# Kernel optimization log

Measured on AMD Instinct MI355X. Metric: run time of the kernel, lower is better.

Reference implementation:

```python
import jax, jax.numpy as jnp
import numpy as np

N_USERS = 100000
N_ITEMS = 50000
NNZ = 1600000
DIM = 128


def setup_inputs() -> dict:
    key = jax.random.key(0)
    ks = jax.random.split(key, 6)
    user_emb = jax.random.normal(ks[0], (N_USERS, DIM), dtype=jnp.float32)
    item_emb = jax.random.normal(ks[1], (N_ITEMS, DIM), dtype=jnp.float32)
    hg_rows = jax.random.randint(ks[2], (NNZ,), 0, N_USERS, dtype=jnp.int32)
    hg_cols = jax.random.randint(ks[3], (NNZ,), 0, N_ITEMS, dtype=jnp.int32)
    hg_vals = jax.random.uniform(ks[4], (NNZ,), dtype=jnp.float32)
    # aggregation: nn.Linear(2*dim, dim) -> weight [dim, 2*dim], bias [dim]
    bound = 1.0 / np.sqrt(2 * DIM)
    W_agg = jax.random.uniform(ks[5], (DIM, 2 * DIM), minval=-bound, maxval=bound, dtype=jnp.float32)
    b_agg = jnp.zeros((DIM,), dtype=jnp.float32)
    return {"user_emb": user_emb, "item_emb": item_emb, "hg_rows": hg_rows,
            "hg_cols": hg_cols, "hg_vals": hg_vals, "W_agg": W_agg, "b_agg": b_agg}


def reference(user_emb, item_emb, hg_rows, hg_cols, hg_vals, W_agg, b_agg):
    n_users = user_emb.shape[0]
    n_items = item_emb.shape[0]
    # node_msg = H @ item_emb  (SpMM via gather + segment_sum)  [n_users, dim]
    gathered = hg_vals[:, None] * item_emb[hg_cols]          # [nnz, dim]
    node_msg = jax.ops.segment_sum(gathered, hg_rows, num_segments=n_users)
    # elementwise gate with user embedding
    edge_node_element = node_msg * user_emb                   # [n_users, dim]
    # msg = Linear(concat([node_msg, gated]))
    cat = jnp.concatenate([node_msg, edge_node_element], axis=1)  # [n_users, 2*dim]
    msg = cat @ W_agg.T + b_agg                               # [n_users, dim]
    # norm_emb = H.T @ msg  (transpose SpMM scatter-back)     [n_items, dim]
    scattered = hg_vals[:, None] * msg[hg_rows]               # [nnz, dim]
    norm_emb = jax.ops.segment_sum(scattered, hg_cols, num_segments=n_items)
    return (norm_emb, msg)
```

## Files before the change

kernel.cpp:

```cpp
#include <hip/hip_runtime.h>

#define DIM 128
#define NB 512

typedef short v8s __attribute__((ext_vector_type(8)));
typedef float v4f __attribute__((ext_vector_type(4)));

__device__ __forceinline__ unsigned short f2bf(float f) {
    unsigned int x = __float_as_uint(f);
    unsigned int r = ((x >> 16) & 1u) + 0x7fffu;
    return (unsigned short)((x + r) >> 16);
}
__device__ __forceinline__ float bf2f(short s) {
    return __uint_as_float(((unsigned)(unsigned short)s) << 16);
}


__global__ __launch_bounds__(256) void k_binA(const int* __restrict__ rows, const int* __restrict__ cols,
                                              int* __restrict__ Mu, int* __restrict__ Mi,
                                              int nnz, int chunk, int nbu, int nbi, int shu, int shi)
{
    __shared__ int hu[256], hi[256];
    int k = blockIdx.x, t = threadIdx.x;
    for (int j = t; j < nbu; j += 256) hu[j] = 0;
    for (int j = t; j < nbi; j += 256) hi[j] = 0;
    __syncthreads();
    int beg = k * chunk, end = min(beg + chunk, nnz);
    if (beg < end) {
        int beg4 = beg >> 2, end4 = end >> 2;
        for (int e4 = beg4 + t; e4 < end4; e4 += 256) {
            int4 r = reinterpret_cast<const int4*>(rows)[e4];
            int4 c = reinterpret_cast<const int4*>(cols)[e4];
            atomicAdd(&hu[r.x >> shu], 1); atomicAdd(&hu[r.y >> shu], 1);
            atomicAdd(&hu[r.z >> shu], 1); atomicAdd(&hu[r.w >> shu], 1);
            atomicAdd(&hi[c.x >> shi], 1); atomicAdd(&hi[c.y >> shi], 1);
            atomicAdd(&hi[c.z >> shi], 1); atomicAdd(&hi[c.w >> shi], 1);
        }
        for (int e = (end4 << 2) + t; e < end; e += 256) {
            atomicAdd(&hu[rows[e] >> shu], 1);
            atomicAdd(&hi[cols[e] >> shi], 1);
        }
    }
    __syncthreads();
    for (int j = t; j < nbu; j += 256) Mu[k * nbu + j] = hu[j];
    for (int j = t; j < nbi; j += 256) Mi[k * nbi + j] = hi[j];
}

__global__ __launch_bounds__(256) void k_binS1(int* __restrict__ M, int* __restrict__ tot,
                                               int nb, int nblk)
{
    __shared__ int ps[256];
    int j = blockIdx.x, t = threadIdx.x;
    int i0 = 2 * t, i1 = 2 * t + 1;
    int v0 = (i0 < nblk) ? M[i0 * nb + j] : 0;
    int v1 = (i1 < nblk) ? M[i1 * nb + j] : 0;
    ps[t] = v0 + v1;
    __syncthreads();
    for (int off = 1; off < 256; off <<= 1) {
        int x = (t >= off) ? ps[t - off] : 0;
        __syncthreads();
        ps[t] += x;
        __syncthreads();
    }
    int ep = ps[t] - (v0 + v1);
    if (i0 < nblk) M[i0 * nb + j] = ep;
    if (i1 < nblk) M[i1 * nb + j] = ep + v0;
    if (t == 255) tot[j] = ps[255];
}

__global__ __launch_bounds__(256) void k_binS2(const int* __restrict__ tot, int* __restrict__ base, int nb)
{
    __shared__ int s[256];
    int t = threadIdx.x;
    int v = (t < nb) ? tot[t] : 0;
    s[t] = v;
    __syncthreads();
    for (int off = 1; off < 256; off <<= 1) {
        int x = (t >= off) ? s[t - off] : 0;
        __syncthreads();
        s[t] += x;
        __syncthreads();
    }
    if (t < nb) base[t] = s[t] - v;
    if (t == 255) base[nb] = s[255];
}

__global__ __launch_bounds__(256) void k_binB(const int* __restrict__ rows, const int* __restrict__ cols,
                                              const float* __restrict__ vals,
                                              const int* __restrict__ Mu, const int* __restrict__ Mi,
                                              const int* __restrict__ base_u, const int* __restrict__ base_i,
                                              int2* __restrict__ bu, int2* __restrict__ bi,
                                              int nnz, int chunk, int nbu, int nbi, int shu, int shi)
{
    __shared__ int cu[256], ci[256];
    int k = blockIdx.x, t = threadIdx.x;
    for (int j = t; j < nbu; j += 256) cu[j] = Mu[k * nbu + j] + base_u[j];
    for (int j = t; j < nbi; j += 256) ci[j] = Mi[k * nbi + j] + base_i[j];
    __syncthreads();
    int mu = (1 << shu) - 1, mi = (1 << shi) - 1;
    int beg = k * chunk, end = min(beg + chunk, nnz);
    if (beg >= end) return;
    int beg4 = beg >> 2, end4 = end >> 2;
    for (int e4 = beg4 + t; e4 < end4; e4 += 256) {
        int4 r = reinterpret_cast<const int4*>(rows)[e4];
        int4 c = reinterpret_cast<const int4*>(cols)[e4];
        int4 v = reinterpret_cast<const int4*>(vals)[e4];
        int p;
        p = atomicAdd(&cu[r.x >> shu], 1); bu[p] = make_int2((c.x << shu) | (r.x & mu), v.x);
        p = atomicAdd(&ci[c.x >> shi], 1); bi[p] = make_int2((r.x << shi) | (c.x & mi), v.x);
        p = atomicAdd(&cu[r.y >> shu], 1); bu[p] = make_int2((c.y << shu) | (r.y & mu), v.y);
        p = atomicAdd(&ci[c.y >> shi], 1); bi[p] = make_int2((r.y << shi) | (c.y & mi), v.y);
        p = atomicAdd(&cu[r.z >> shu], 1); bu[p] = make_int2((c.z << shu) | (r.z & mu), v.z);
        p = atomicAdd(&ci[c.z >> shi], 1); bi[p] = make_int2((r.z << shi) | (c.z & mi), v.z);
        p = atomicAdd(&cu[r.w >> shu], 1); bu[p] = make_int2((c.w << shu) | (r.w & mu), v.w);
        p = atomicAdd(&ci[c.w >> shi], 1); bi[p] = make_int2((r.w << shi) | (c.w & mi), v.w);
    }
    for (int e = (end4 << 2) + t; e < end; e += 256) {
        int r = rows[e], c = cols[e];
        int v = reinterpret_cast<const int*>(vals)[e];
        int p;
        p = atomicAdd(&cu[r >> shu], 1); bu[p] = make_int2((c << shu) | (r & mu), v);
        p = atomicAdd(&ci[c >> shi], 1); bi[p] = make_int2((r << shi) | (c & mi), v);
    }
}

__global__ __launch_bounds__(256) void k_binC(const int2* __restrict__ binned,
                                              const int* __restrict__ base,
                                              int* __restrict__ ptr, int2* __restrict__ cs,
                                              int nrows, int sh, int total)
{
    __shared__ int hist[512];
    __shared__ int scn[512];
    __shared__ int psum[256];
    int j = blockIdx.x, t = threadIdx.x;
    int BR = 1 << sh;
    int row0 = j << sh;
    int beg = base[j], end = base[j + 1];
    for (int r = t; r < BR; r += 256) hist[r] = 0;
    __syncthreads();
    for (int e = beg + t; e < end; e += 256)
        atomicAdd(&hist[binned[e].x & (BR - 1)], 1);
    __syncthreads();
    int v0 = (2 * t < BR) ? hist[2 * t] : 0;
    int v1 = (2 * t + 1 < BR) ? hist[2 * t + 1] : 0;
    psum[t] = v0 + v1;
    __syncthreads();
    for (int off = 1; off < 256; off <<= 1) {
        int x = (t >= off) ? psum[t - off] : 0;
        __syncthreads();
        psum[t] += x;
        __syncthreads();
    }
    int ep = psum[t] - (v0 + v1);
    if (2 * t < BR) scn[2 * t] = ep;
    if (2 * t + 1 < BR) scn[2 * t + 1] = ep + v0;
    __syncthreads();
    for (int r = t; r < BR; r += 256) {
        int row = row0 + r;
        if (row < nrows) ptr[row] = beg + scn[r];
        hist[r] = 0;
    }
    if (j == 0 && t == 0) ptr[nrows] = total;
    __syncthreads();
    for (int e = beg + t; e < end; e += 256) {
        int2 rec = binned[e];
        int rl = rec.x & (BR - 1);
        int pos = beg + scn[rl] + atomicAdd(&hist[rl], 1);
        cs[pos] = make_int2(((unsigned)rec.x) >> sh, rec.y);
    }
}

__global__ void k_tobf(const float* __restrict__ in, unsigned short* __restrict__ out, int n8)
{
    int i = blockIdx.x * 256 + threadIdx.x;
    if (i >= n8) return;
    float4 a = reinterpret_cast<const float4*>(in)[2 * i];
    float4 c = reinterpret_cast<const float4*>(in)[2 * i + 1];
    uint4 o;
    o.x = (unsigned)f2bf(a.x) | ((unsigned)f2bf(a.y) << 16);
    o.y = (unsigned)f2bf(a.z) | ((unsigned)f2bf(a.w) << 16);
    o.z = (unsigned)f2bf(c.x) | ((unsigned)f2bf(c.y) << 16);
    o.w = (unsigned)f2bf(c.z) | ((unsigned)f2bf(c.w) << 16);
    reinterpret_cast<uint4*>(out)[i] = o;
}

__device__ __forceinline__ void gather8(const int2* __restrict__ pairs,
                                        const unsigned short* __restrict__ src,
                                        int beg, int end, int lr, int gb,
                                        float* __restrict__ acc)
{
    for (int base = beg; base < end; base += 8) {
        int2 pl = make_int2(0, 0);
        if (lr < 8 && base + lr < end) pl = pairs[base + lr];
        int   idx[8];
        float vv[8];
        #pragma unroll
        for (int e = 0; e < 8; ++e) {
            idx[e] = __shfl(pl.x, gb + e, 64);
            vv[e]  = __int_as_float(__shfl(pl.y, gb + e, 64));
        }
        v8s s[8];
        #pragma unroll
        for (int e = 0; e < 8; ++e)
            s[e] = *reinterpret_cast<const v8s*>(src + (long long)idx[e] * DIM + 8 * lr);
        #pragma unroll
        for (int e = 0; e < 8; ++e) {
            #pragma unroll
            for (int k = 0; k < 8; ++k)
                acc[k] += vv[e] * bf2f(s[e][k]);
        }
    }
}

__global__ __launch_bounds__(256) void k_spmm_bf(const int* __restrict__ ptr, const int2* __restrict__ pairs,
                                                 const unsigned short* __restrict__ src,
                                                 float* __restrict__ dst, int nrows)
{
    int r = blockIdx.x * 16 + (threadIdx.x >> 4);
    if (r >= nrows) return;
    int lr = threadIdx.x & 15;
    int gb = (threadIdx.x & 63) & ~15;
    int beg = ptr[r], end = ptr[r + 1];
    float acc[8];
    #pragma unroll
    for (int k = 0; k < 8; ++k) acc[k] = 0.f;
    gather8(pairs, src, beg, end, lr, gb, acc);
    float4 o0, o1;
    o0.x = acc[0]; o0.y = acc[1]; o0.z = acc[2]; o0.w = acc[3];
    o1.x = acc[4]; o1.y = acc[5]; o1.z = acc[6]; o1.w = acc[7];
    float* dp = dst + (long long)r * DIM + 8 * lr;
    *reinterpret_cast<float4*>(dp) = o0;
    *reinterpret_cast<float4*>(dp + 4) = o1;
}

__global__ __launch_bounds__(256) void k_spmm4(const int* __restrict__ ptr, const int2* __restrict__ pairs,
                                               const float* __restrict__ src, float* __restrict__ dst, int nrows)
{
    int r = blockIdx.x * 8 + (threadIdx.x >> 5);
    if (r >= nrows) return;
    int l = threadIdx.x & 31;
    int beg = ptr[r], end = ptr[r + 1];
    float4 a0 = {0.f, 0.f, 0.f, 0.f}, a1 = {0.f, 0.f, 0.f, 0.f};
    int j = beg;
    for (; j + 1 < end; j += 2) {
        int2 p0 = pairs[j], p1 = pairs[j + 1];
        float v0 = __int_as_float(p0.y), v1 = __int_as_float(p1.y);
        float4 s0 = *reinterpret_cast<const float4*>(src + (long long)p0.x * DIM + 4 * l);
        float4 s1 = *reinterpret_cast<const float4*>(src + (long long)p1.x * DIM + 4 * l);
        a0.x += v0 * s0.x; a0.y += v0 * s0.y; a0.z += v0 * s0.z; a0.w += v0 * s0.w;
        a1.x += v1 * s1.x; a1.y += v1 * s1.y; a1.z += v1 * s1.z; a1.w += v1 * s1.w;
    }
    if (j < end) {
        int2 p0 = pairs[j];
        float v0 = __int_as_float(p0.y);
        float4 s0 = *reinterpret_cast<const float4*>(src + (long long)p0.x * DIM + 4 * l);
        a0.x += v0 * s0.x; a0.y += v0 * s0.y; a0.z += v0 * s0.z; a0.w += v0 * s0.w;
    }
    a0.x += a1.x; a0.y += a1.y; a0.z += a1.z; a0.w += a1.w;
    *reinterpret_cast<float4*>(dst + (long long)r * DIM + 4 * l) = a0;
}

__global__ void k_bsw(const float* __restrict__ W, unsigned short* __restrict__ Bsw)
{
    int i = blockIdx.x * 256 + threadIdx.x;
    int kt = i >> 12;
    int rem = i & 4095;
    int c = rem >> 5;
    int kk = rem & 31;
    Bsw[i] = f2bf(W[c * 256 + kt * 32 + kk]);
}

__global__ __launch_bounds__(256) void k_fused(const int* __restrict__ ptr,
                                               const int2* __restrict__ pairs,
                                               const unsigned short* __restrict__ itbf,
                                               const float* __restrict__ ue,
                                               const unsigned short* __restrict__ Bsw,
                                               const float* __restrict__ b,
                                               float* __restrict__ msg,
                                               unsigned short* __restrict__ msg_bf, int nu)
{
    __shared__ unsigned short cat[4][16 * 264];
    int tid = threadIdx.x;
    int w = tid >> 6, l = tid & 63;
    int lr = l & 15, hi = l >> 4;
    int gb = l & ~15;
    int d = lr * 8;
    int uw = blockIdx.x * 64 + w * 16;
    unsigned short* mycat = &cat[w][0];

    #pragma unroll
    for (int p = 0; p < 4; ++p) {
        int ur = p * 4 + hi;
        int u = uw + ur;
        float acc[8];
        #pragma unroll
        for (int k = 0; k < 8; ++k) acc[k] = 0.f;
        float4 ue0 = make_float4(0.f,0.f,0.f,0.f), ue1 = make_float4(0.f,0.f,0.f,0.f);
        if (u < nu) {
            ue0 = *reinterpret_cast<const float4*>(ue + (long long)u * DIM + d);
            ue1 = *reinterpret_cast<const float4*>(ue + (long long)u * DIM + d + 4);
            int beg = ptr[u], end = ptr[u + 1];
            gather8(pairs, itbf, beg, end, lr, gb, acc);
        }
        float uev[8] = {ue0.x, ue0.y, ue0.z, ue0.w, ue1.x, ue1.y, ue1.z, ue1.w};
        uint4 nmp, gp;
        nmp.x = (unsigned)f2bf(acc[0]) | ((unsigned)f2bf(acc[1]) << 16);
        nmp.y = (unsigned)f2bf(acc[2]) | ((unsigned)f2bf(acc[3]) << 16);
        nmp.z = (unsigned)f2bf(acc[4]) | ((unsigned)f2bf(acc[5]) << 16);
        nmp.w = (unsigned)f2bf(acc[6]) | ((unsigned)f2bf(acc[7]) << 16);
        gp.x = (unsigned)f2bf(acc[0] * uev[0]) | ((unsigned)f2bf(acc[1] * uev[1]) << 16);
        gp.y = (unsigned)f2bf(acc[2] * uev[2]) | ((unsigned)f2bf(acc[3] * uev[3]) << 16);
        gp.z = (unsigned)f2bf(acc[4] * uev[4]) | ((unsigned)f2bf(acc[5] * uev[5]) << 16);
        gp.w = (unsigned)f2bf(acc[6] * uev[6]) | ((unsigned)f2bf(acc[7] * uev[7]) << 16);
        *reinterpret_cast<uint4*>(mycat + ur * 264 + d) = nmp;
        *reinterpret_cast<uint4*>(mycat + ur * 264 + 128 + d) = gp;
    }
    __syncthreads();

    v4f facc[8];
    #pragma unroll
    for (int ct = 0; ct < 8; ++ct) facc[ct] = (v4f){0.f, 0.f, 0.f, 0.f};
    const unsigned short* arow = mycat + lr * 264;
    for (int kt = 0; kt < 8; ++kt) {
        v8s a = *reinterpret_cast<const v8s*>(arow + kt * 32 + hi * 8);
        #pragma unroll
        for (int ct = 0; ct < 8; ++ct) {
            v8s bb = *reinterpret_cast<const v8s*>(Bsw + kt * 4096 + (ct * 16 + lr) * 32 + hi * 8);
            facc[ct] = __builtin_amdgcn_mfma_f32_16x16x32_bf16(a, bb, facc[ct], 0, 0, 0);
        }
    }

    int ub = uw + hi * 4;
    #pragma unroll
    for (int ct = 0; ct < 8; ++ct) {
        float bc = b[ct * 16 + lr];
        #pragma unroll
        for (int j = 0; j < 4; ++j) {
            int u = ub + j;
            if (u < nu) {
                float val = facc[ct][j] + bc;
                long long p = (long long)u * DIM + ct * 16 + lr;
                msg[p] = val;
                msg_bf[p] = f2bf(val);
            }
        }
    }
}

__global__ __launch_bounds__(256) void k_msg5(const float* __restrict__ nm_in,
                                              const float* __restrict__ ue,
                                              const unsigned short* __restrict__ Bsw,
                                              const float* __restrict__ b,
                                              float* __restrict__ msg,
                                              unsigned short* __restrict__ msg_bf, int nu)
{
    __shared__ unsigned short cat[64 * 264];
    int tid = threadIdx.x;
    int u0 = blockIdx.x * 64;

    for (int idx = tid; idx < 2048; idx += 256) {
        int u = idx >> 5, d4 = idx & 31;
        float4 nm4 = make_float4(0.f, 0.f, 0.f, 0.f);
        float4 ue4 = make_float4(0.f, 0.f, 0.f, 0.f);
        if (u0 + u < nu) {
            long long p = (long long)(u0 + u) * DIM + d4 * 4;
            nm4 = *reinterpret_cast<const float4*>(nm_in + p);
            ue4 = *reinterpret_cast<const float4*>(ue + p);
        }
        unsigned short* row = cat + u * 264;
        uint2 nmp, gp;
        nmp.x = (unsigned)f2bf(nm4.x) | ((unsigned)f2bf(nm4.y) << 16);
        nmp.y = (unsigned)f2bf(nm4.z) | ((unsigned)f2bf(nm4.w) << 16);
        gp.x  = (unsigned)f2bf(nm4.x * ue4.x) | ((unsigned)f2bf(nm4.y * ue4.y) << 16);
        gp.y  = (unsigned)f2bf(nm4.z * ue4.z) | ((unsigned)f2bf(nm4.w * ue4.w) << 16);
        *reinterpret_cast<uint2*>(row + d4 * 4) = nmp;
        *reinterpret_cast<uint2*>(row + 128 + d4 * 4) = gp;
    }
    __syncthreads();

    int l = tid & 63, w = tid >> 6;
    int lr = l & 15, hi = l >> 4;
    v4f acc[8];
    #pragma unroll
    for (int ct = 0; ct < 8; ++ct) acc[ct] = (v4f){0.f, 0.f, 0.f, 0.f};

    const unsigned short* arow = cat + (w * 16 + lr) * 264;
    for (int kt = 0; kt < 8; ++kt) {
        v8s a = *reinterpret_cast<const v8s*>(arow + kt * 32 + hi * 8);
        #pragma unroll
        for (int ct = 0; ct < 8; ++ct) {
            v8s bb = *reinterpret_cast<const v8s*>(Bsw + kt * 4096 + (ct * 16 + lr) * 32 + hi * 8);
            acc[ct] = __builtin_amdgcn_mfma_f32_16x16x32_bf16(a, bb, acc[ct], 0, 0, 0);
        }
    }

    int ub = u0 + w * 16 + hi * 4;
    #pragma unroll
    for (int ct = 0; ct < 8; ++ct) {
        float bc = b[ct * 16 + lr];
        #pragma unroll
        for (int j = 0; j < 4; ++j) {
            int u = ub + j;
            if (u < nu) {
                float val = acc[ct][j] + bc;
                long long p = (long long)u * DIM + ct * 16 + lr;
                msg[p] = val;
                msg_bf[p] = f2bf(val);
            }
        }
    }
}

__global__ void k_wt(const float* __restrict__ W, float* __restrict__ Wt)
{
    int t = blockIdx.x * 256 + threadIdx.x;
    int k = t >> 7;
    int c = t & 127;
    Wt[t] = W[c * 256 + k];
}

#define UPB 32
#define CATP 260

__global__ __launch_bounds__(256) void k_msg4(const float* __restrict__ nm_in,
                                              const float* __restrict__ ue,
                                              const float* __restrict__ Wt,
                                              const float* __restrict__ b,
                                              float* __restrict__ msg, int nu)
{
    __shared__ float cat[UPB * CATP];
    int tid = threadIdx.x;
    int u0 = blockIdx.x * UPB;
    for (int idx = tid; idx < UPB * DIM; idx += 256) {
        int u = idx >> 7, d = idx & 127;
        float nm = 0.f, g = 0.f;
        if (u0 + u < nu) {
            long long p = (long long)(u0 + u) * DIM + d;
            nm = nm_in[p];
            g = nm * ue[p];
        }
        cat[u * CATP + d] = nm;
        cat[u * CATP + DIM + d] = g;
    }
    __syncthreads();

    int tc = tid & 31;
    int tu = tid >> 5;
    float acc[4][4];
    #pragma unroll
    for (int r = 0; r < 4; ++r)
        #pragma unroll
        for (int c = 0; c < 4; ++c) acc[r][c] = 0.f;

    const float* cbase = &cat[(tu * 4) * CATP];
    for (int k4 = 0; k4 < 64; ++k4) {
        float4 w[4];
        #pragma unroll
        for (int kk = 0; kk < 4; ++kk)
            w[kk] = *reinterpret_cast<const float4*>(Wt + (k4 * 4 + kk) * DIM + tc * 4);
        #pragma unroll
        for (int r = 0; r < 4; ++r) {
            float4 a = *reinterpret_cast<const float4*>(cbase + r * CATP + k4 * 4);
            acc[r][0] += a.x * w[0].x + a.y * w[1].x + a.z * w[2].x + a.w * w[3].x;
            acc[r][1] += a.x * w[0].y + a.y * w[1].y + a.z * w[2].y + a.w * w[3].y;
            acc[r][2] += a.x * w[0].z + a.y * w[1].z + a.z * w[2].z + a.w * w[3].z;
            acc[r][3] += a.x * w[0].w + a.y * w[1].w + a.z * w[2].w + a.w * w[3].w;
        }
    }

    float4 bb = *reinterpret_cast<const float4*>(b + tc * 4);
    #pragma unroll
    for (int r = 0; r < 4; ++r) {
        int u = u0 + tu * 4 + r;
        if (u < nu) {
            float4 o;
            o.x = acc[r][0] + bb.x; o.y = acc[r][1] + bb.y;
            o.z = acc[r][2] + bb.z; o.w = acc[r][3] + bb.w;
            *reinterpret_cast<float4*>(msg + (long long)u * DIM + tc * 4) = o;
        }
    }
}


__global__ void k_count(const int* __restrict__ rows, const int* __restrict__ cols,
                        int* __restrict__ cnt_u, int* __restrict__ cnt_i, int nnz4, int nnz)
{
    int i = blockIdx.x * blockDim.x + threadIdx.x;
    int stride = gridDim.x * blockDim.x;
    for (int e4 = i; e4 < nnz4; e4 += stride) {
        int4 r = reinterpret_cast<const int4*>(rows)[e4];
        int4 c = reinterpret_cast<const int4*>(cols)[e4];
        atomicAdd(&cnt_u[r.x], 1); atomicAdd(&cnt_u[r.y], 1);
        atomicAdd(&cnt_u[r.z], 1); atomicAdd(&cnt_u[r.w], 1);
        atomicAdd(&cnt_i[c.x], 1); atomicAdd(&cnt_i[c.y], 1);
        atomicAdd(&cnt_i[c.z], 1); atomicAdd(&cnt_i[c.w], 1);
    }
    for (int e = nnz4 * 4 + i; e < nnz; e += stride) {
        atomicAdd(&cnt_u[rows[e]], 1);
        atomicAdd(&cnt_i[cols[e]], 1);
    }
}

__global__ void k_scan1(const int* __restrict__ cnt, int* __restrict__ ptr,
                        int* __restrict__ partial, int n)
{
    __shared__ int s[256];
    int i = blockIdx.x * 256 + threadIdx.x;
    int v = (i < n) ? cnt[i] : 0;
    s[threadIdx.x] = v;
    __syncthreads();
    for (int off = 1; off < 256; off <<= 1) {
        int x = (threadIdx.x >= off) ? s[threadIdx.x - off] : 0;
        __syncthreads();
        s[threadIdx.x] += x;
        __syncthreads();
    }
    if (i < n) ptr[i] = s[threadIdx.x] - v;
    if (threadIdx.x == 255) partial[blockIdx.x] = s[255];
}

__global__ void k_scan2(int* __restrict__ partial, int n)
{
    __shared__ int s[512];
    int v = (threadIdx.x < (unsigned)n) ? partial[threadIdx.x] : 0;
    s[threadIdx.x] = v;
    __syncthreads();
    for (int off = 1; off < 512; off <<= 1) {
        int x = (threadIdx.x >= off) ? s[threadIdx.x - off] : 0;
        __syncthreads();
        s[threadIdx.x] += x;
        __syncthreads();
    }
    if (threadIdx.x < (unsigned)n) partial[threadIdx.x] = s[threadIdx.x] - v;
}

__global__ void k_scan3(int* __restrict__ ptr, const int* __restrict__ partial,
                        int* __restrict__ woff, int n, int total)
{
    int i = blockIdx.x * 256 + threadIdx.x;
    if (i < n) {
        int p = ptr[i] + partial[blockIdx.x];
        ptr[i] = p;
        woff[i] = p;
        if (i == n - 1) ptr[n] = total;
    }
}

__global__ void k_edge_scatter(const int* __restrict__ rows, const int* __restrict__ cols,
                               const float* __restrict__ vals,
                               int* __restrict__ woff_u, int* __restrict__ woff_i,
                               int2* __restrict__ cs_u, int2* __restrict__ cs_i,
                               int nnz4, int nnz)
{
    int i = blockIdx.x * blockDim.x + threadIdx.x;
    int stride = gridDim.x * blockDim.x;
    for (int e4 = i; e4 < nnz4; e4 += stride) {
        int4 r = reinterpret_cast<const int4*>(rows)[e4];
        int4 c = reinterpret_cast<const int4*>(cols)[e4];
        float4 v = reinterpret_cast<const float4*>(vals)[e4];
        int pu, pi;
        pu = atomicAdd(&woff_u[r.x], 1); cs_u[pu] = make_int2(c.x, __float_as_int(v.x));
        pi = atomicAdd(&woff_i[c.x], 1); cs_i[pi] = make_int2(r.x, __float_as_int(v.x));
        pu = atomicAdd(&woff_u[r.y], 1); cs_u[pu] = make_int2(c.y, __float_as_int(v.y));
        pi = atomicAdd(&woff_i[c.y], 1); cs_i[pi] = make_int2(r.y, __float_as_int(v.y));
        pu = atomicAdd(&woff_u[r.z], 1); cs_u[pu] = make_int2(c.z, __float_as_int(v.z));
        pi = atomicAdd(&woff_i[c.z], 1); cs_i[pi] = make_int2(r.z, __float_as_int(v.z));
        pu = atomicAdd(&woff_u[r.w], 1); cs_u[pu] = make_int2(c.w, __float_as_int(v.w));
        pi = atomicAdd(&woff_i[c.w], 1); cs_i[pi] = make_int2(r.w, __float_as_int(v.w));
    }
    for (int e = nnz4 * 4 + i; e < nnz; e += stride) {
        int r = rows[e], c = cols[e];
        float v = vals[e];
        int pu = atomicAdd(&woff_u[r], 1); cs_u[pu] = make_int2(c, __float_as_int(v));
        int pi = atomicAdd(&woff_i[c], 1); cs_i[pi] = make_int2(r, __float_as_int(v));
    }
}


__global__ void k_scatter(const int* __restrict__ didx, const int* __restrict__ sidx,
                          const float* __restrict__ vals, const float* __restrict__ src,
                          float* __restrict__ dst, long long nnz)
{
    long long t = (long long)blockIdx.x * blockDim.x + threadIdx.x;
    long long total = nnz * 32;
    if (t >= total) return;
    long long e = t >> 5;
    int d = (int)(t & 31) * 4;
    int si = sidx[e];
    int di = didx[e];
    float v = vals[e];
    const float4 s = *reinterpret_cast<const float4*>(src + (long long)si * DIM + d);
    float* p = dst + (long long)di * DIM + d;
    atomicAdd(p + 0, v * s.x);
    atomicAdd(p + 1, v * s.y);
    atomicAdd(p + 2, v * s.z);
    atomicAdd(p + 3, v * s.w);
}

__global__ void k_msg_simple(const float* __restrict__ user_emb, const float* __restrict__ W,
                             const float* __restrict__ b, float* __restrict__ msg)
{
    __shared__ float cat[2 * DIM];
    int u = blockIdx.x;
    int t = threadIdx.x;
    long long base = (long long)u * DIM;
    float nm = msg[base + t];
    float ue = user_emb[base + t];
    cat[t] = nm;
    cat[DIM + t] = nm * ue;
    __syncthreads();
    float acc = b[t];
    const float4* Wr = reinterpret_cast<const float4*>(W + (long long)t * 2 * DIM);
    const float4* c4 = reinterpret_cast<const float4*>(cat);
    #pragma unroll
    for (int k = 0; k < 2 * DIM / 4; ++k) {
        float4 w = Wr[k];
        float4 c = c4[k];
        acc += w.x * c.x + w.y * c.y + w.z * c.z + w.w * c.w;
    }
    msg[base + t] = acc;
}


extern "C" void kernel_launch(void* const* d_in, const int* in_sizes, int n_in,
                              void* d_out, int out_size, void* d_ws, size_t ws_size,
                              hipStream_t stream) {
    const float* user_emb = (const float*)d_in[0];
    const float* item_emb = (const float*)d_in[1];
    const int*   rows     = (const int*)d_in[2];
    const int*   cols     = (const int*)d_in[3];
    const float* vals     = (const float*)d_in[4];
    const float* W        = (const float*)d_in[5];
    const float* b        = (const float*)d_in[6];

    int nu = in_sizes[0] / DIM;
    int ni = in_sizes[1] / DIM;
    int nnz = in_sizes[2];

    float* norm_emb = (float*)d_out;
    float* msg      = (float*)d_out + (long long)ni * DIM;

    auto align256 = [](size_t x) { return (x + 255) & ~(size_t)255; };

    int shu = 0; while ((((long long)nu + (1LL << shu) - 1) >> shu) > 256) shu++;
    int shi = 0; while ((((long long)ni + (1LL << shi) - 1) >> shi) > 256) shi++;
    int nbu = (int)(((long long)nu + (1LL << shu) - 1) >> shu);
    int nbi = (int)(((long long)ni + (1LL << shi) - 1) >> shi);
    int chunk = (((nnz + NB - 1) / NB) + 3) & ~3;

    size_t off = 0;
    size_t o_bu    = off; off = align256(off + (size_t)nnz * 8);
    size_t o_bi    = off; off = align256(off + (size_t)nnz * 8);
    size_t o_csu   = off; off = align256(off + (size_t)nnz * 8);
    size_t o_Mu    = off; off = align256(off + (size_t)NB * nbu * 4);
    size_t o_Mi    = off; off = align256(off + (size_t)NB * nbi * 4);
    size_t o_totu  = off; off = align256(off + (size_t)nbu * 4);
    size_t o_toti  = off; off = align256(off + (size_t)nbi * 4);
    size_t o_baseu = off; off = align256(off + (size_t)(nbu + 1) * 4);
    size_t o_basei = off; off = align256(off + (size_t)(nbi + 1) * 4);
    size_t o_ptru  = off; off = align256(off + (size_t)(nu + 1) * 4);
    size_t o_ptri  = off; off = align256(off + (size_t)(ni + 1) * 4);
    size_t o_bsw   = off; off = align256(off + (size_t)32768 * 2);
    size_t need_base = off;

    size_t itbf_need  = (size_t)ni * DIM * 2;
    size_t msgbf_need = (size_t)nu * DIM * 2;
    bool alias_it = (o_csu - o_bi) >= itbf_need;

    size_t need_fused = need_base;
    size_t o_msgbf_f = need_fused; need_fused = align256(need_fused + msgbf_need);
    size_t o_itbf_f;
    if (alias_it) o_itbf_f = o_bi;
    else { o_itbf_f = need_fused; need_fused = align256(need_fused + itbf_need); }

    size_t need_r9 = need_base;
    bool alias_msg = (o_Mu - o_bi) >= msgbf_need;
    size_t o_itbf_9, o_msgbf_9;
    if (alias_it) o_itbf_9 = o_bi;
    else { o_itbf_9 = need_r9; need_r9 = align256(need_r9 + itbf_need); }
    if (alias_msg) o_msgbf_9 = o_bi;
    else { o_msgbf_9 = need_r9; need_r9 = align256(need_r9 + msgbf_need); }

    bool pack_ok = ((long long)ni < (1LL << (31 - shu))) && ((long long)nu < (1LL << (31 - shi)))
                   && (shu <= 9) && (shi <= 9);

    off = 0;
    size_t o_cs_u   = off; off = align256(off + (size_t)nnz * 8);
    size_t o_cs_i   = off; off = align256(off + (size_t)nnz * 8);
    size_t o_ptr_u  = off; off = align256(off + (size_t)(nu + 1) * 4);
    size_t o_ptr_i  = off; off = align256(off + (size_t)(ni + 1) * 4);
    size_t o_woff_u = off; off = align256(off + (size_t)nu * 4);
    size_t o_woff_i = off; off = align256(off + (size_t)ni * 4);
    size_t o_part_u = off; off = align256(off + 512 * 4);
    size_t o_part_i = off; off = align256(off + 512 * 4);
    size_t o_wt2    = off; off = align256(off + (size_t)256 * DIM * 4);
    size_t need_r5 = off;

    int npb_u = (nu + 255) / 256;
    int npb_i = (ni + 255) / 256;

    char* ws = (char*)d_ws;

    if (pack_ok && (ws_size >= need_fused || ws_size >= need_r9)) {
        bool fused = (ws_size >= need_fused);
        int2* bu     = (int2*)(ws + o_bu);
        int2* bi     = (int2*)(ws + o_bi);
        int2* cs_u   = (int2*)(ws + o_csu);
        int2* cs_i   = (int2*)(ws + o_bu);
        int*  Mu     = (int*)(ws + o_Mu);
        int*  Mi     = (int*)(ws + o_Mi);
        int*  totu   = (int*)(ws + o_totu);
        int*  toti   = (int*)(ws + o_toti);
        int*  baseu  = (int*)(ws + o_baseu);
        int*  basei  = (int*)(ws + o_basei);
        int*  ptr_u  = (int*)(ws + o_ptru);
        int*  ptr_i  = (int*)(ws + o_ptri);
        unsigned short* bsw   = (unsigned short*)(ws + o_bsw);
        unsigned short* itbf  = (unsigned short*)(ws + (fused ? o_itbf_f : o_itbf_9));
        unsigned short* msgbf = (unsigned short*)(ws + (fused ? o_msgbf_f : o_msgbf_9));

        k_binA<<<NB, 256, 0, stream>>>(rows, cols, Mu, Mi, nnz, chunk, nbu, nbi, shu, shi);
        k_bsw<<<128, 256, 0, stream>>>(W, bsw);
        k_binS1<<<nbu, 256, 0, stream>>>(Mu, totu, nbu, NB);
        k_binS1<<<nbi, 256, 0, stream>>>(Mi, toti, nbi, NB);
        k_binS2<<<1, 256, 0, stream>>>(totu, baseu, nbu);
        k_binS2<<<1, 256, 0, stream>>>(toti, basei, nbi);
        k_binB<<<NB, 256, 0, stream>>>(rows, cols, vals, Mu, Mi, baseu, basei,
                                       bu, bi, nnz, chunk, nbu, nbi, shu, shi);
        k_binC<<<nbu, 256, 0, stream>>>(bu, baseu, ptr_u, cs_u, nu, shu, nnz);
        k_binC<<<nbi, 256, 0, stream>>>(bi, basei, ptr_i, cs_i, ni, shi, nnz);

        int n8i = ni * DIM / 8;
        k_tobf<<<(n8i + 255) / 256, 256, 0, stream>>>(item_emb, itbf, n8i);

        if (fused) {
            k_fused<<<(nu + 63) / 64, 256, 0, stream>>>(ptr_u, cs_u, itbf, user_emb,
                                                        bsw, b, msg, msgbf, nu);
        } else {
            k_spmm_bf<<<(nu + 15) / 16, 256, 0, stream>>>(ptr_u, cs_u, itbf, msg, nu);
            k_msg5<<<(nu + 63) / 64, 256, 0, stream>>>(msg, user_emb, bsw, b, msg, msgbf, nu);
        }
        k_spmm_bf<<<(ni + 15) / 16, 256, 0, stream>>>(ptr_i, cs_i, msgbf, norm_emb, ni);
    } else if (ws_size >= need_r5 && npb_u <= 512 && npb_i <= 512) {
        int2*  cs_u   = (int2*)(ws + o_cs_u);
        int2*  cs_i   = (int2*)(ws + o_cs_i);
        int*   ptr_u  = (int*)(ws + o_ptr_u);
        int*   ptr_i  = (int*)(ws + o_ptr_i);
        int*   woff_u = (int*)(ws + o_woff_u);
        int*   woff_i = (int*)(ws + o_woff_i);
        int*   part_u = (int*)(ws + o_part_u);
        int*   part_i = (int*)(ws + o_part_i);
        float* wt     = (float*)(ws + o_wt2);

        hipMemsetAsync(woff_u, 0, (size_t)nu * 4, stream);
        hipMemsetAsync(woff_i, 0, (size_t)ni * 4, stream);

        int nnz4 = nnz / 4;
        int gs = 1024;
        k_count<<<gs, 256, 0, stream>>>(rows, cols, woff_u, woff_i, nnz4, nnz);
        k_wt<<<(256 * DIM) / 256, 256, 0, stream>>>(W, wt);

        k_scan1<<<npb_u, 256, 0, stream>>>(woff_u, ptr_u, part_u, nu);
        k_scan1<<<npb_i, 256, 0, stream>>>(woff_i, ptr_i, part_i, ni);
        k_scan2<<<1, 512, 0, stream>>>(part_u, npb_u);
        k_scan2<<<1, 512, 0, stream>>>(part_i, npb_i);
        k_scan3<<<npb_u, 256, 0, stream>>>(ptr_u, part_u, woff_u, nu, nnz);
        k_scan3<<<npb_i, 256, 0, stream>>>(ptr_i, part_i, woff_i, ni, nnz);

        k_edge_scatter<<<gs, 256, 0, stream>>>(rows, cols, vals, woff_u, woff_i,
                                               cs_u, cs_i, nnz4, nnz);

        k_spmm4<<<(nu + 7) / 8, 256, 0, stream>>>(ptr_u, cs_u, item_emb, msg, nu);
        k_msg4<<<(nu + UPB - 1) / UPB, 256, 0, stream>>>(msg, user_emb, wt, b, msg, nu);
        k_spmm4<<<(ni + 7) / 8, 256, 0, stream>>>(ptr_i, cs_i, msg, norm_emb, ni);
    } else {
        hipMemsetAsync(d_out, 0, (size_t)out_size * sizeof(float), stream);
        long long tot = (long long)nnz * 32;
        int blk = 256;
        long long nblk = (tot + blk - 1) / blk;
        k_scatter<<<(int)nblk, blk, 0, stream>>>(rows, cols, vals, item_emb, msg, nnz);
        k_msg_simple<<<nu, DIM, 0, stream>>>(user_emb, W, b, msg);
        k_scatter<<<(int)nblk, blk, 0, stream>>>(cols, rows, vals, msg, norm_emb, nnz);
    }
}
```

Measured before the change: 266.8 us.

## Gather 16 neighbors per iteration, shrink fused block, pre-convert user embeddings to bf16

The gather helper now loads 16 (index, value) pairs per iteration, using all 16 lanes of each row group, and issues two batches of 8 loads. This halves the loop trips and shuffle overhead per edge. The fused kernel now runs 128-thread blocks covering 32 users, which halves its shared memory and adds more blocks. A new pass converts user embeddings to bf16 in workspace so the fused kernel reads half the bytes, at the cost of an extra full read and write of user_emb and lower gate precision.

```diff
diff --git a/kernel.cpp b/kernel.cpp
--- a/kernel.cpp
+++ b/kernel.cpp
@@ -184,18 +184,18 @@
     reinterpret_cast<uint4*>(out)[i] = o;
 }
 
-__device__ __forceinline__ void gather8(const int2* __restrict__ pairs,
-                                        const unsigned short* __restrict__ src,
-                                        int beg, int end, int lr, int gb,
-                                        float* __restrict__ acc)
-{
-    for (int base = beg; base < end; base += 8) {
+__device__ __forceinline__ void gather16(const int2* __restrict__ pairs,
+                                         const unsigned short* __restrict__ src,
+                                         int beg, int end, int lr, int gb,
+                                         float* __restrict__ acc)
+{
+    for (int base = beg; base < end; base += 16) {
         int2 pl = make_int2(0, 0);
-        if (lr < 8 && base + lr < end) pl = pairs[base + lr];
-        int   idx[8];
-        float vv[8];
-        #pragma unroll
-        for (int e = 0; e < 8; ++e) {
+        if (base + lr < end) pl = pairs[base + lr];
+        int   idx[16];
+        float vv[16];
+        #pragma unroll
+        for (int e = 0; e < 16; ++e) {
             idx[e] = __shfl(pl.x, gb + e, 64);
             vv[e]  = __int_as_float(__shfl(pl.y, gb + e, 64));
         }
@@ -208,6 +208,15 @@
             #pragma unroll
             for (int k = 0; k < 8; ++k)
                 acc[k] += vv[e] * bf2f(s[e][k]);
+        }
+        #pragma unroll
+        for (int e = 0; e < 8; ++e)
+            s[e] = *reinterpret_cast<const v8s*>(src + (long long)idx[8 + e] * DIM + 8 * lr);
+        #pragma unroll
+        for (int e = 0; e < 8; ++e) {
+            #pragma unroll
+            for (int k = 0; k < 8; ++k)
+                acc[k] += vv[8 + e] * bf2f(s[e][k]);
         }
     }
 }
@@ -224,7 +233,7 @@
     float acc[8];
     #pragma unroll
     for (int k = 0; k < 8; ++k) acc[k] = 0.f;
-    gather8(pairs, src, beg, end, lr, gb, acc);
+    gather16(pairs, src, beg, end, lr, gb, acc);
     float4 o0, o1;
     o0.x = acc[0]; o0.y = acc[1]; o0.z = acc[2]; o0.w = acc[3];
     o1.x = acc[4]; o1.y = acc[5]; o1.z = acc[6]; o1.w = acc[7];
@@ -270,22 +279,24 @@
     Bsw[i] = f2bf(W[c * 256 + kt * 32 + kk]);
 }
 
-__global__ __launch_bounds__(256) void k_fused(const int* __restrict__ ptr,
+__global__ __launch_bounds__(128) void k_fused(const int* __restrict__ ptr,
                                                const int2* __restrict__ pairs,
                                                const unsigned short* __restrict__ itbf,
-                                               const float* __restrict__ ue,
+                                               const float* __restrict__ uef32,
+                                               const unsigned short* __restrict__ uebf,
+                                               int use_uebf,
                                                const unsigned short* __restrict__ Bsw,
                                                const float* __restrict__ b,
                                                float* __restrict__ msg,
                                                unsigned short* __restrict__ msg_bf, int nu)
 {
-    __shared__ unsigned short cat[4][16 * 264];
+    __shared__ unsigned short cat[2][16 * 264];
     int tid = threadIdx.x;
     int w = tid >> 6, l = tid & 63;
     int lr = l & 15, hi = l >> 4;
     int gb = l & ~15;
     int d = lr * 8;
-    int uw = blockIdx.x * 64 + w * 16;
+    int uw = blockIdx.x * 32 + w * 16;
     unsigned short* mycat = &cat[w][0];
 
     #pragma unroll
@@ -295,14 +306,25 @@
         float acc[8];
         #pragma unroll
         for (int k = 0; k < 8; ++k) acc[k] = 0.f;
-        float4 ue0 = make_float4(0.f,0.f,0.f,0.f), ue1 = make_float4(0.f,0.f,0.f,0.f);
+        float uev[8];
+        #pragma unroll
+        for (int k = 0; k < 8; ++k) uev[k] = 0.f;
         if (u < nu) {
-            ue0 = *reinterpret_cast<const float4*>(ue + (long long)u * DIM + d);
-            ue1 = *reinterpret_cast<const float4*>(ue + (long long)u * DIM + d + 4);
+            if (use_uebf) {
+                uint4 up = *reinterpret_cast<const uint4*>(uebf + (long long)u * DIM + d);
+                uev[0] = bf2f((short)(up.x & 0xffff)); uev[1] = bf2f((short)(up.x >> 16));
+                uev[2] = bf2f((short)(up.y & 0xffff)); uev[3] = bf2f((short)(up.y >> 16));
+                uev[4] = bf2f((short)(up.z & 0xffff)); uev[5] = bf2f((short)(up.z >> 16));
+                uev[6] = bf2f((short)(up.w & 0xffff)); uev[7] = bf2f((short)(up.w >> 16));
+            } else {
+                float4 ue0 = *reinterpret_cast<const float4*>(uef32 + (long long)u * DIM + d);
+                float4 ue1 = *reinterpret_cast<const float4*>(uef32 + (long long)u * DIM + d + 4);
+                uev[0] = ue0.x; uev[1] = ue0.y; uev[2] = ue0.z; uev[3] = ue0.w;
+                uev[4] = ue1.x; uev[5] = ue1.y; uev[6] = ue1.z; uev[7] = ue1.w;
+            }
             int beg = ptr[u], end = ptr[u + 1];
-            gather8(pairs, itbf, beg, end, lr, gb, acc);
-        }
-        float uev[8] = {ue0.x, ue0.y, ue0.z, ue0.w, ue1.x, ue1.y, ue1.z, ue1.w};
+            gather16(pairs, itbf, beg, end, lr, gb, acc);
+        }
         uint4 nmp, gp;
         nmp.x = (unsigned)f2bf(acc[0]) | ((unsigned)f2bf(acc[1]) << 16);
         nmp.y = (unsigned)f2bf(acc[2]) | ((unsigned)f2bf(acc[3]) << 16);
@@ -665,6 +687,7 @@
 
     size_t itbf_need  = (size_t)ni * DIM * 2;
     size_t msgbf_need = (size_t)nu * DIM * 2;
+    size_t uebf_need  = (size_t)nu * DIM * 2;
     bool alias_it = (o_csu - o_bi) >= itbf_need;
 
     size_t need_fused = need_base;
@@ -672,6 +695,8 @@
     size_t o_itbf_f;
     if (alias_it) o_itbf_f = o_bi;
     else { o_itbf_f = need_fused; need_fused = align256(need_fused + itbf_need); }
+    size_t o_uebf = need_fused;
+    size_t need_fused_ue = align256(need_fused + uebf_need);
 
     size_t need_r9 = need_base;
     bool alias_msg = (o_Mu - o_bi) >= msgbf_need;
@@ -702,7 +727,8 @@
     char* ws = (char*)d_ws;
 
     if (pack_ok && (ws_size >= need_fused || ws_size >= need_r9)) {
-        bool fused = (ws_size >= need_fused);
+        bool fused   = (ws_size >= need_fused);
+        bool use_ue  = fused && (ws_size >= need_fused_ue);
         int2* bu     = (int2*)(ws + o_bu);
         int2* bi     = (int2*)(ws + o_bi);
         int2* cs_u   = (int2*)(ws + o_csu);
@@ -718,9 +744,14 @@
         unsigned short* bsw   = (unsigned short*)(ws + o_bsw);
         unsigned short* itbf  = (unsigned short*)(ws + (fused ? o_itbf_f : o_itbf_9));
         unsigned short* msgbf = (unsigned short*)(ws + (fused ? o_msgbf_f : o_msgbf_9));
+        unsigned short* uebf  = (unsigned short*)(ws + o_uebf);
 
         k_binA<<<NB, 256, 0, stream>>>(rows, cols, Mu, Mi, nnz, chunk, nbu, nbi, shu, shi);
         k_bsw<<<128, 256, 0, stream>>>(W, bsw);
+        if (use_ue) {
+            int n8u = nu * DIM / 8;
+            k_tobf<<<(n8u + 255) / 256, 256, 0, stream>>>(user_emb, uebf, n8u);
+        }
         k_binS1<<<nbu, 256, 0, stream>>>(Mu, totu, nbu, NB);
         k_binS1<<<nbi, 256, 0, stream>>>(Mi, toti, nbi, NB);
         k_binS2<<<1, 256, 0, stream>>>(totu, baseu, nbu);
@@ -734,7 +765,8 @@
         k_tobf<<<(n8i + 255) / 256, 256, 0, stream>>>(item_emb, itbf, n8i);
 
         if (fused) {
-            k_fused<<<(nu + 63) / 64, 256, 0, stream>>>(ptr_u, cs_u, itbf, user_emb,
+            k_fused<<<(nu + 31) / 32, 128, 0, stream>>>(ptr_u, cs_u, itbf, user_emb,
+                                                        uebf, use_ue ? 1 : 0,
                                                         bsw, b, msg, msgbf, nu);
         } else {
             k_spmm_bf<<<(nu + 15) / 16, 256, 0, stream>>>(ptr_u, cs_u, itbf, msg, nu);
```

Measured after the change: 285.6 us. +7.0%, slower.
